# Kernel tuning notes

Measured on AMD Instinct MI355X. Metric: run time of the kernel, lower is better.

## Reference

```python
import jax, jax.numpy as jnp
import numpy as np

H = 1024
S = 8192
B = 1  # module's broadcast in the weighted-sum step only supports B == 1


def setup_inputs() -> dict:
    key = jax.random.key(0)
    k1, k2, k3 = jax.random.split(key, 3)
    scale = 1.0 / np.sqrt(H)
    enc_out = jax.random.normal(k1, (B, S, H), dtype=jnp.float32)
    w1 = jax.random.normal(k2, (H, H), dtype=jnp.float32) * scale  # nn.Linear weight [out,in]
    w2 = jax.random.normal(k3, (H, H), dtype=jnp.float32) * scale
    return {"enc_out": enc_out, "w1": w1, "w2": w2}


def reference(enc_out, w1, w2):
    # attn_weights = tanh(w1(enc_out)) @ w2(enc_out)^T  -> [B, S, S]
    q = jnp.tanh(jnp.einsum('bsh,oh->bso', enc_out, w1))
    k = jnp.einsum('bsh,oh->bso', enc_out, w2)
    scores = jnp.einsum('bih,bjh->bij', q, k)          # [B, S, S]
    attn = jax.nn.softmax(scores, axis=1)               # softmax over dim=1 (rows)
    # torch: sum over dim=1 of attn[B,S,S,1] * enc_out broadcast as [1,B,S,H].
    # For B==1 this equals enc_out[0,j,h] * sum_i attn[0,i,j]; avoid the
    # [B,S,S,H] intermediate the eager torch code materializes.
    col_sum = jnp.sum(attn, axis=1)                     # [B, S]
    context = col_sum[..., None] * enc_out              # [B, S, H]
    return context, attn
```

## Files before the change

### kernel.cpp

```cpp
#include <hip/hip_runtime.h>
#include <hip/hip_bf16.h>
#include <math.h>


typedef _Float16 half_t;
typedef _Float16 half8 __attribute__((ext_vector_type(8)));
typedef _Float16 half4 __attribute__((ext_vector_type(4)));
typedef float f32x4 __attribute__((ext_vector_type(4)));

#define S_DIM 8192
#define H_DIM 1024

__device__ __forceinline__ void gload16(const void* g, void* l) {
  __builtin_amdgcn_global_load_lds(
      (const __attribute__((address_space(1))) void*)g,
      (__attribute__((address_space(3))) void*)l, 16, 0, 0);
}

#define WAITVM(N) asm volatile("s_waitcnt vmcnt(" #N ")" ::: "memory")

__global__ void __launch_bounds__(256) k_cvt(const float* __restrict__ src,
                                             half_t* __restrict__ dst) {
  long g = (long)blockIdx.x * 256 + threadIdx.x;
  f32x4 x = ((const f32x4*)src)[g];
  half4 h;
#pragma unroll
  for (int e = 0; e < 4; ++e) h[e] = (half_t)x[e];
  ((half4*)dst)[g] = h;
}

#define GEMM_MAINLOOP_256(APTR, BPTR)                                          \
  __shared__ __align__(16) half_t As[4][8192];                                 \
  __shared__ __align__(16) half_t Bs[4][8192];                                 \
  const int tid = threadIdx.x;                                                 \
  const int lane = tid & 63;                                                   \
  const int quad = lane >> 4;                                                  \
  const int l15 = lane & 15;                                                   \
  const int wave = tid >> 6;                                                   \
  const int wm = wave >> 2;                                          \
  const int wn = wave & 3;                                           \
  int aoff[2], boff[2], loff[2];                                               \
  _Pragma("unroll") for (int t = 0; t < 2; ++t) {                              \
    int f8 = t * 512 + tid;                                       \
    int u = f8 >> 8;                                                 \
    int m = f8 & 255;                                                          \
    aoff[t] = (bm * 256 + m) * H_DIM + u * 8;                                  \
    boff[t] = (bn * 256 + m) * H_DIM + u * 8;                                  \
    loff[t] = f8 * 8;                                                          \
  }                                                                            \
  f32x4 acc[8][4];                                                             \
  _Pragma("unroll") for (int r = 0; r < 8; ++r)                                \
      _Pragma("unroll") for (int c = 0; c < 4; ++c)                            \
          acc[r][c] = (f32x4){0.f, 0.f, 0.f, 0.f};                             \
               \
  _Pragma("unroll") for (int pc = 0; pc < 3; ++pc)                             \
      _Pragma("unroll") for (int t = 0; t < 2; ++t) {                          \
    gload16(APTR + aoff[t] + pc * 32, &As[pc][loff[t]]);                       \
    gload16(BPTR + boff[t] + pc * 32, &Bs[pc][loff[t]]);                       \
  }                                                                            \
  const int abase = (quad * 256 + wm * 128 + l15) * 8;                         \
  const int bbase = (quad * 256 + wn * 64 + l15) * 8;                          \
  _Pragma("unroll 1") for (int ch = 0; ch < 32; ++ch) {                        \
    const int buf = ch & 3;                                                    \
    if (ch <= 29) { WAITVM(8); }           \
    else if (ch == 30) { WAITVM(4); }                                          \
    else { WAITVM(0); }                                                        \
    __builtin_amdgcn_s_barrier();                                              \
    asm volatile("" ::: "memory");        \
    if (ch + 3 < 32) {  \
      const int nb = (ch + 3) & 3;                                             \
      _Pragma("unroll") for (int t = 0; t < 2; ++t) {                          \
        gload16(APTR + aoff[t] + (ch + 3) * 32, &As[nb][loff[t]]);             \
        gload16(BPTR + boff[t] + (ch + 3) * 32, &Bs[nb][loff[t]]);             \
      }                                                                        \
    }                                                                          \
    half8 af[8], bf[4];                                                        \
    _Pragma("unroll") for (int r = 0; r < 8; ++r)                              \
        af[r] = *(const half8*)&As[buf][abase + r * 128];                      \
    _Pragma("unroll") for (int c = 0; c < 4; ++c)                              \
        bf[c] = *(const half8*)&Bs[buf][bbase + c * 128];                      \
    __builtin_amdgcn_s_setprio(1);                                             \
    _Pragma("unroll") for (int r = 0; r < 8; ++r)                              \
        _Pragma("unroll") for (int c = 0; c < 4; ++c)                          \
            acc[r][c] = __builtin_amdgcn_mfma_f32_16x16x32_f16(                \
                af[r], bf[c], acc[r][c], 0, 0, 0);                             \
    __builtin_amdgcn_s_setprio(0);                                             \
  }

__global__ void __launch_bounds__(512, 2) k_gemm_qk(const half_t* __restrict__ A,
                                                    const half_t* __restrict__ B,
                                                    half_t* __restrict__ Qh,
                                                    half_t* __restrict__ Kh) {
  const int bm = blockIdx.y;
  const int bn = blockIdx.x;
  GEMM_MAINLOOP_256(A, B)
  const int colb = bn * 256 + wn * 64;
  const int rowb = bm * 256 + wm * 128;
  const bool isQ = (bn < 4);
#pragma unroll
  for (int r = 0; r < 8; ++r) {
#pragma unroll
    for (int c = 0; c < 4; ++c) {
      int col = colb + c * 16 + l15;
      int row = rowb + r * 16 + quad * 4;
      if (isQ) {
#pragma unroll
        for (int v = 0; v < 4; ++v)
          Qh[(long)(row + v) * 1024 + col] = (half_t)tanhf(acc[r][c][v]);
      } else {
#pragma unroll
        for (int v = 0; v < 4; ++v)
          Kh[(long)(row + v) * 1024 + (col - 1024)] = (half_t)acc[r][c][v];
      }
    }
  }
}

template <bool FUSE_STATS>
__global__ void __launch_bounds__(512, 2) k_gemm_scores(const half_t* __restrict__ A,
                                                        const half_t* __restrict__ B,
                                                        float* __restrict__ out,
                                                        float* __restrict__ Pm,
                                                        float* __restrict__ Ps) {
  const int lin = blockIdx.x;
  const int patch = lin >> 6;
  const int local = lin & 63;
  const int bm = (patch >> 2) * 8 + (local >> 3);
  const int bn = (patch & 3) * 8 + (local & 7);
  GEMM_MAINLOOP_256(A, B)
  const int colb = bn * 256 + wn * 64;
  const int rowb = bm * 256 + wm * 128;
#pragma unroll
  for (int r = 0; r < 8; ++r) {
#pragma unroll
    for (int c = 0; c < 4; ++c) {
      int col = colb + c * 16 + l15;
      int row = rowb + r * 16 + quad * 4;
#pragma unroll
      for (int v = 0; v < 4; ++v) {
        out[(long)(row + v) * S_DIM + col] = acc[r][c][v];
      }
    }
  }
  if (FUSE_STATS) {
    float cmax[4], csum[4];
#pragma unroll
    for (int c = 0; c < 4; ++c) {
      float m = acc[0][c][0];
#pragma unroll
      for (int r = 0; r < 8; ++r)
#pragma unroll
        for (int v = 0; v < 4; ++v) m = fmaxf(m, acc[r][c][v]);
      m = fmaxf(m, __shfl_xor(m, 16, 64));
      m = fmaxf(m, __shfl_xor(m, 32, 64));
      cmax[c] = m;
      float s = 0.f;
#pragma unroll
      for (int r = 0; r < 8; ++r)
#pragma unroll
        for (int v = 0; v < 4; ++v) s += __expf(acc[r][c][v] - m);
      s += __shfl_xor(s, 16, 64);
      s += __shfl_xor(s, 32, 64);
      csum[c] = s;
    }
    float* sred = (float*)As;
    if (quad == 0) {
#pragma unroll
      for (int c = 0; c < 4; ++c) {
        int idx = (((wm * 4 + wn) * 4 + c) * 16 + l15) * 2;
        sred[idx] = cmax[c];
        sred[idx + 1] = csum[c];
      }
    }
    __syncthreads();
    if (wm == 0 && quad == 0) {
#pragma unroll
      for (int c = 0; c < 4; ++c) {
        int i0 = (((0 * 4 + wn) * 4 + c) * 16 + l15) * 2;
        int i1 = (((1 * 4 + wn) * 4 + c) * 16 + l15) * 2;
        float m0 = sred[i0], s0 = sred[i0 + 1];
        float m1 = sred[i1], s1 = sred[i1 + 1];
        float M = fmaxf(m0, m1);
        float Ssum = s0 * __expf(m0 - M) + s1 * __expf(m1 - M);
        int col = colb + c * 16 + l15;
        Pm[(long)bm * S_DIM + col] = M;
        Ps[(long)bm * S_DIM + col] = Ssum;
      }
    }
  }
}

__global__ void __launch_bounds__(256) k_colstats(const float* __restrict__ P,
                                                  float* __restrict__ Pm,
                                                  float* __restrict__ Ps) {
  const int c = threadIdx.x & 63;
  const int rg = threadIdx.x >> 6;
  const int j = blockIdx.x * 64 + c;
  const int seg = blockIdx.y;
  float m = -3.0e38f, s = 0.f;
  for (int t = 0; t < 256; ++t) {
    int i = seg * 1024 + t * 4 + rg;
    float x = P[(long)i * S_DIM + j];
    float mn = fmaxf(m, x);
    s = s * __expf(m - mn) + __expf(x - mn);
    m = mn;
  }
  __shared__ float sm[4][64];
  __shared__ float ss[4][64];
  sm[rg][c] = m;
  ss[rg][c] = s;
  __syncthreads();
  if (threadIdx.x < 64) {
    float mm = sm[0][c];
#pragma unroll
    for (int r = 1; r < 4; ++r) mm = fmaxf(mm, sm[r][c]);
    float sum = 0.f;
#pragma unroll
    for (int r = 0; r < 4; ++r) sum += ss[r][c] * __expf(sm[r][c] - mm);
    Pm[seg * S_DIM + j] = mm;
    Ps[seg * S_DIM + j] = sum;
  }
}

__global__ void __launch_bounds__(256) k_combine(const float* __restrict__ Pm,
                                                 const float* __restrict__ Ps,
                                                 float* __restrict__ Mcol,
                                                 float* __restrict__ Rcol,
                                                 int nseg) {
  int j = blockIdx.x * 256 + threadIdx.x;
  float m = Pm[j];
  for (int r = 1; r < nseg; ++r) m = fmaxf(m, Pm[(long)r * S_DIM + j]);
  float s = 0.f;
  for (int r = 0; r < nseg; ++r)
    s += Ps[(long)r * S_DIM + j] * __expf(Pm[(long)r * S_DIM + j] - m);
  Mcol[j] = m;
  Rcol[j] = 1.0f / s;
}

__global__ void __launch_bounds__(256) k_norm(float* __restrict__ P,
                                              const float* __restrict__ Mcol,
                                              const float* __restrict__ Rcol,
                                              const f32x4* __restrict__ enc,
                                              f32x4* __restrict__ ctx) {
  long b = blockIdx.x;
  if (b >= 65536) {
    long g = (b - 65536) * 256 + threadIdx.x;
    ctx[g] = enc[g];
    return;
  }
  long gid = b * 256 + threadIdx.x;
  int j4 = (int)(gid & 2047);
  f32x4 x = ((const f32x4*)P)[gid];
  f32x4 a = ((const f32x4*)Mcol)[j4];
  f32x4 r = ((const f32x4*)Rcol)[j4];
  f32x4 o;
#pragma unroll
  for (int e = 0; e < 4; ++e) o[e] = __expf(x[e] - a[e]) * r[e];
  ((f32x4*)P)[gid] = o;
}

extern "C" void kernel_launch(void* const* d_in, const int* in_sizes, int n_in,
                              void* d_out, int out_size, void* d_ws, size_t ws_size,
                              hipStream_t stream) {
  const float* enc = (const float*)d_in[0];
  const float* w1 = (const float*)d_in[1];
  const float* w2 = (const float*)d_in[2];

  float* out = (float*)d_out;
  float* ctx = out;
  float* attn = out + 8388608;

  half_t* Qh = (half_t*)ctx;
  half_t* Kh = Qh + 8388608;
  half_t* enc_h = (half_t*)attn;
  half_t* w_h = (half_t*)((char*)attn + 16777216);

  const bool fuse = ws_size >= (size_t)(32 + 32 + 2) * S_DIM * 4;
  const int nseg = fuse ? 32 : 8;
  char* ws = (char*)d_ws;
  float* Pm = (float*)ws;
  float* Ps = (float*)(ws + (size_t)nseg * S_DIM * 4);
  float* Mcol = (float*)(ws + (size_t)2 * nseg * S_DIM * 4);
  float* Rcol = Mcol + S_DIM;

  k_cvt<<<8192, 256, 0, stream>>>(enc, enc_h);
  k_cvt<<<1024, 256, 0, stream>>>(w1, w_h);
  k_cvt<<<1024, 256, 0, stream>>>(w2, w_h + 1048576);

  k_gemm_qk<<<dim3(8, 32), 512, 0, stream>>>(enc_h, w_h, Qh, Kh);

  if (fuse) {
    k_gemm_scores<true><<<1024, 512, 0, stream>>>(Qh, Kh, attn, Pm, Ps);
  } else {
    k_gemm_scores<false><<<1024, 512, 0, stream>>>(Qh, Kh, attn, Pm, Ps);
    k_colstats<<<dim3(128, 8), 256, 0, stream>>>(attn, Pm, Ps);
  }
  k_combine<<<32, 256, 0, stream>>>(Pm, Ps, Mcol, Rcol, nseg);

  k_norm<<<73728, 256, 0, stream>>>(attn, Mcol, Rcol, (const f32x4*)enc,
                                    (f32x4*)ctx);
}
```

Before: 785.7 us.

## Recompute score GEMM instead of materializing scores, and split mainloop into phases

```diff
diff --git a/kernel.cpp b/kernel.cpp
--- a/kernel.cpp
+++ b/kernel.cpp
@@ -1,5 +1,4 @@
 #include <hip/hip_runtime.h>
-#include <hip/hip_bf16.h>
 #include <math.h>
 
 
@@ -18,6 +17,12 @@
 }
 
 #define WAITVM(N) asm volatile("s_waitcnt vmcnt(" #N ")" ::: "memory")
+#define BAR()                      \
+  do {                             \
+    asm volatile("" ::: "memory"); \
+    __builtin_amdgcn_s_barrier();  \
+    asm volatile("" ::: "memory"); \
+  } while (0)
 
 __global__ void __launch_bounds__(256) k_cvt(const float* __restrict__ src,
                                              half_t* __restrict__ dst) {
@@ -29,7 +34,7 @@
   ((half4*)dst)[g] = h;
 }
 
-#define GEMM_MAINLOOP_256(APTR, BPTR)                                          \
+#define GEMM_MAINLOOP_8PH(APTR, BPTR)                                          \
   __shared__ __align__(16) half_t As[4][8192];                                 \
   __shared__ __align__(16) half_t Bs[4][8192];                                 \
   const int tid = threadIdx.x;                                                 \
@@ -41,50 +46,69 @@
   const int wn = wave & 3;                                           \
   int aoff[2], boff[2], loff[2];                                               \
   _Pragma("unroll") for (int t = 0; t < 2; ++t) {                              \
-    int f8 = t * 512 + tid;                                       \
-    int u = f8 >> 8;                                                 \
-    int m = f8 & 255;                                                          \
+    int f = t * 512 + tid;                                        \
+    int u = f >> 8;                                                  \
+    int m = f & 255;                                                           \
     aoff[t] = (bm * 256 + m) * H_DIM + u * 8;                                  \
     boff[t] = (bn * 256 + m) * H_DIM + u * 8;                                  \
-    loff[t] = f8 * 8;                                                          \
+    loff[t] = f * 8;                                                           \
   }                                                                            \
   f32x4 acc[8][4];                                                             \
   _Pragma("unroll") for (int r = 0; r < 8; ++r)                                \
       _Pragma("unroll") for (int c = 0; c < 4; ++c)                            \
           acc[r][c] = (f32x4){0.f, 0.f, 0.f, 0.f};                             \
-               \
-  _Pragma("unroll") for (int pc = 0; pc < 3; ++pc)                             \
-      _Pragma("unroll") for (int t = 0; t < 2; ++t) {                          \
-    gload16(APTR + aoff[t] + pc * 32, &As[pc][loff[t]]);                       \
-    gload16(BPTR + boff[t] + pc * 32, &Bs[pc][loff[t]]);                       \
+                      \
+  _Pragma("unroll") for (int pg = 0; pg < 3; ++pg) {                           \
+    _Pragma("unroll") for (int t = 0; t < 2; ++t)                              \
+        gload16(APTR + aoff[t] + pg * 32, &As[pg][loff[t]]);                   \
+    _Pragma("unroll") for (int t = 0; t < 2; ++t)                              \
+        gload16(BPTR + boff[t] + pg * 32, &Bs[pg][loff[t]]);                   \
   }                                                                            \
-  const int abase = (quad * 256 + wm * 128 + l15) * 8;                         \
-  const int bbase = (quad * 256 + wn * 64 + l15) * 8;                          \
-  _Pragma("unroll 1") for (int ch = 0; ch < 32; ++ch) {                        \
-    const int buf = ch & 3;                                                    \
-    if (ch <= 29) { WAITVM(8); }           \
-    else if (ch == 30) { WAITVM(4); }                                          \
-    else { WAITVM(0); }                                                        \
-    __builtin_amdgcn_s_barrier();                                              \
-    asm volatile("" ::: "memory");        \
-    if (ch + 3 < 32) {  \
-      const int nb = (ch + 3) & 3;                                             \
-      _Pragma("unroll") for (int t = 0; t < 2; ++t) {                          \
-        gload16(APTR + aoff[t] + (ch + 3) * 32, &As[nb][loff[t]]);             \
-        gload16(BPTR + boff[t] + (ch + 3) * 32, &Bs[nb][loff[t]]);             \
-      }                                                                        \
+  WAITVM(4);               \
+  BAR();                                                                       \
+  const int arow = (quad * 256 + wm * 128 + l15) * 8;                          \
+  const int brow = (quad * 256 + wn * 64 + l15) * 8;                           \
+  _Pragma("unroll 1") for (int g = 0; g < 32; ++g) {                           \
+    const half_t* Asl = As[g & 3];                                             \
+    const half_t* Bsl = Bs[g & 3];                                             \
+    half8 af[4], bf[4];                                                        \
+                             \
+    _Pragma("unroll") for (int r = 0; r < 4; ++r)                              \
+        af[r] = *(const half8*)&Asl[arow + r * 128];                           \
+    _Pragma("unroll") for (int c = 0; c < 4; ++c)                              \
+        bf[c] = *(const half8*)&Bsl[brow + c * 128];                           \
+    if (g + 3 < 32) {                 \
+      const int ns = (g + 3) & 3;                                              \
+      _Pragma("unroll") for (int t = 0; t < 2; ++t)                            \
+          gload16(APTR + aoff[t] + (g + 3) * 32, &As[ns][loff[t]]);            \
     }                                                                          \
-    half8 af[8], bf[4];                                                        \
-    _Pragma("unroll") for (int r = 0; r < 8; ++r)                              \
-        af[r] = *(const half8*)&As[buf][abase + r * 128];                      \
-    _Pragma("unroll") for (int c = 0; c < 4; ++c)                              \
-        bf[c] = *(const half8*)&Bs[buf][bbase + c * 128];                      \
+    BAR();                                                                     \
     __builtin_amdgcn_s_setprio(1);                                             \
-    _Pragma("unroll") for (int r = 0; r < 8; ++r)                              \
+    _Pragma("unroll") for (int r = 0; r < 4; ++r)                              \
         _Pragma("unroll") for (int c = 0; c < 4; ++c)                          \
             acc[r][c] = __builtin_amdgcn_mfma_f32_16x16x32_f16(                \
                 af[r], bf[c], acc[r][c], 0, 0, 0);                             \
     __builtin_amdgcn_s_setprio(0);                                             \
+    BAR();                                                                     \
+                   \
+    _Pragma("unroll") for (int r = 0; r < 4; ++r)                              \
+        af[r] = *(const half8*)&Asl[arow + (r + 4) * 128];                     \
+    if (g + 3 < 32) {                                   \
+      const int ns = (g + 3) & 3;                                              \
+      _Pragma("unroll") for (int t = 0; t < 2; ++t)                            \
+          gload16(BPTR + boff[t] + (g + 3) * 32, &Bs[ns][loff[t]]);            \
+    }                                                                          \
+    BAR();                                                                     \
+    __builtin_amdgcn_s_setprio(1);                                             \
+    _Pragma("unroll") for (int r = 0; r < 4; ++r)                              \
+        _Pragma("unroll") for (int c = 0; c < 4; ++c)                          \
+            acc[r + 4][c] = __builtin_amdgcn_mfma_f32_16x16x32_f16(            \
+                af[r], bf[c], acc[r + 4][c], 0, 0, 0);                         \
+    __builtin_amdgcn_s_setprio(0);                                             \
+    if (g & 1) {           \
+      if (g < 27) { WAITVM(4); } else { WAITVM(0); }                           \
+    }                                                                          \
+    BAR();                                                                     \
   }
 
 __global__ void __launch_bounds__(512, 2) k_gemm_qk(const half_t* __restrict__ A,
@@ -93,7 +117,7 @@
                                                     half_t* __restrict__ Kh) {
   const int bm = blockIdx.y;
   const int bn = blockIdx.x;
-  GEMM_MAINLOOP_256(A, B)
+  GEMM_MAINLOOP_8PH(A, B)
   const int colb = bn * 256 + wn * 64;
   const int rowb = bm * 256 + wm * 128;
   const bool isQ = (bn < 4);
@@ -116,147 +140,110 @@
   }
 }
 
-template <bool FUSE_STATS>
-__global__ void __launch_bounds__(512, 2) k_gemm_scores(const half_t* __restrict__ A,
-                                                        const half_t* __restrict__ B,
-                                                        float* __restrict__ out,
-                                                        float* __restrict__ Pm,
-                                                        float* __restrict__ Ps) {
+__global__ void __launch_bounds__(512, 2) k_stats(const half_t* __restrict__ A,
+                                                  const half_t* __restrict__ B,
+                                                  float* __restrict__ Pm,
+                                                  float* __restrict__ Ps) {
   const int lin = blockIdx.x;
   const int patch = lin >> 6;
   const int local = lin & 63;
   const int bm = (patch >> 2) * 8 + (local >> 3);
   const int bn = (patch & 3) * 8 + (local & 7);
-  GEMM_MAINLOOP_256(A, B)
+  GEMM_MAINLOOP_8PH(A, B)
   const int colb = bn * 256 + wn * 64;
-  const int rowb = bm * 256 + wm * 128;
-#pragma unroll
-  for (int r = 0; r < 8; ++r) {
+  float cmax[4], csum[4];
+#pragma unroll
+  for (int c = 0; c < 4; ++c) {
+    float m = acc[0][c][0];
+#pragma unroll
+    for (int r = 0; r < 8; ++r)
+#pragma unroll
+      for (int v = 0; v < 4; ++v) m = fmaxf(m, acc[r][c][v]);
+    m = fmaxf(m, __shfl_xor(m, 16, 64));
+    m = fmaxf(m, __shfl_xor(m, 32, 64));
+    cmax[c] = m;
+    float s = 0.f;
+#pragma unroll
+    for (int r = 0; r < 8; ++r)
+#pragma unroll
+      for (int v = 0; v < 4; ++v) s += __expf(acc[r][c][v] - m);
+    s += __shfl_xor(s, 16, 64);
+    s += __shfl_xor(s, 32, 64);
+    csum[c] = s;
+  }
+  float* sred = (float*)As;
+  if (quad == 0) {
 #pragma unroll
     for (int c = 0; c < 4; ++c) {
+      int idx = (((wm * 4 + wn) * 4 + c) * 16 + l15) * 2;
+      sred[idx] = cmax[c];
+      sred[idx + 1] = csum[c];
+    }
+  }
+  __syncthreads();
+  if (wm == 0 && quad == 0) {
+#pragma unroll
+    for (int c = 0; c < 4; ++c) {
+      int i0 = (((0 * 4 + wn) * 4 + c) * 16 + l15) * 2;
+      int i1 = (((1 * 4 + wn) * 4 + c) * 16 + l15) * 2;
+      float m0 = sred[i0], s0 = sred[i0 + 1];
+      float m1 = sred[i1], s1 = sred[i1 + 1];
+      float M = fmaxf(m0, m1);
+      float Ssum = s0 * __expf(m0 - M) + s1 * __expf(m1 - M);
       int col = colb + c * 16 + l15;
-      int row = rowb + r * 16 + quad * 4;
-#pragma unroll
-      for (int v = 0; v < 4; ++v) {
-        out[(long)(row + v) * S_DIM + col] = acc[r][c][v];
-      }
-    }
-  }
-  if (FUSE_STATS) {
-    float cmax[4], csum[4];
-#pragma unroll
-    for (int c = 0; c < 4; ++c) {
-      float m = acc[0][c][0];
-#pragma unroll
-      for (int r = 0; r < 8; ++r)
-#pragma unroll
-        for (int v = 0; v < 4; ++v) m = fmaxf(m, acc[r][c][v]);
-      m = fmaxf(m, __shfl_xor(m, 16, 64));
-      m = fmaxf(m, __shfl_xor(m, 32, 64));
-      cmax[c] = m;
-      float s = 0.f;
-#pragma unroll
-      for (int r = 0; r < 8; ++r)
-#pragma unroll
-        for (int v = 0; v < 4; ++v) s += __expf(acc[r][c][v] - m);
-      s += __shfl_xor(s, 16, 64);
-      s += __shfl_xor(s, 32, 64);
-      csum[c] = s;
-    }
-    float* sred = (float*)As;
-    if (quad == 0) {
-#pragma unroll
-      for (int c = 0; c < 4; ++c) {
-        int idx = (((wm * 4 + wn) * 4 + c) * 16 + l15) * 2;
-        sred[idx] = cmax[c];
-        sred[idx + 1] = csum[c];
-      }
-    }
-    __syncthreads();
-    if (wm == 0 && quad == 0) {
-#pragma unroll
-      for (int c = 0; c < 4; ++c) {
-        int i0 = (((0 * 4 + wn) * 4 + c) * 16 + l15) * 2;
-        int i1 = (((1 * 4 + wn) * 4 + c) * 16 + l15) * 2;
-        float m0 = sred[i0], s0 = sred[i0 + 1];
-        float m1 = sred[i1], s1 = sred[i1 + 1];
-        float M = fmaxf(m0, m1);
-        float Ssum = s0 * __expf(m0 - M) + s1 * __expf(m1 - M);
-        int col = colb + c * 16 + l15;
-        Pm[(long)bm * S_DIM + col] = M;
-        Ps[(long)bm * S_DIM + col] = Ssum;
-      }
-    }
-  }
-}
-
-__global__ void __launch_bounds__(256) k_colstats(const float* __restrict__ P,
-                                                  float* __restrict__ Pm,
-                                                  float* __restrict__ Ps) {
-  const int c = threadIdx.x & 63;
-  const int rg = threadIdx.x >> 6;
-  const int j = blockIdx.x * 64 + c;
-  const int seg = blockIdx.y;
-  float m = -3.0e38f, s = 0.f;
-  for (int t = 0; t < 256; ++t) {
-    int i = seg * 1024 + t * 4 + rg;
-    float x = P[(long)i * S_DIM + j];
-    float mn = fmaxf(m, x);
-    s = s * __expf(m - mn) + __expf(x - mn);
-    m = mn;
-  }
-  __shared__ float sm[4][64];
-  __shared__ float ss[4][64];
-  sm[rg][c] = m;
-  ss[rg][c] = s;
-  __syncthreads();
-  if (threadIdx.x < 64) {
-    float mm = sm[0][c];
-#pragma unroll
-    for (int r = 1; r < 4; ++r) mm = fmaxf(mm, sm[r][c]);
-    float sum = 0.f;
-#pragma unroll
-    for (int r = 0; r < 4; ++r) sum += ss[r][c] * __expf(sm[r][c] - mm);
-    Pm[seg * S_DIM + j] = mm;
-    Ps[seg * S_DIM + j] = sum;
+      Pm[(long)bm * S_DIM + col] = M;
+      Ps[(long)bm * S_DIM + col] = Ssum;
+    }
   }
 }
 
 __global__ void __launch_bounds__(256) k_combine(const float* __restrict__ Pm,
                                                  const float* __restrict__ Ps,
                                                  float* __restrict__ Mcol,
-                                                 float* __restrict__ Rcol,
-                                                 int nseg) {
+                                                 float* __restrict__ Rcol) {
   int j = blockIdx.x * 256 + threadIdx.x;
   float m = Pm[j];
-  for (int r = 1; r < nseg; ++r) m = fmaxf(m, Pm[(long)r * S_DIM + j]);
+  for (int r = 1; r < 32; ++r) m = fmaxf(m, Pm[(long)r * S_DIM + j]);
   float s = 0.f;
-  for (int r = 0; r < nseg; ++r)
+  for (int r = 0; r < 32; ++r)
     s += Ps[(long)r * S_DIM + j] * __expf(Pm[(long)r * S_DIM + j] - m);
   Mcol[j] = m;
   Rcol[j] = 1.0f / s;
 }
 
-__global__ void __launch_bounds__(256) k_norm(float* __restrict__ P,
-                                              const float* __restrict__ Mcol,
-                                              const float* __restrict__ Rcol,
-                                              const f32x4* __restrict__ enc,
-                                              f32x4* __restrict__ ctx) {
-  long b = blockIdx.x;
-  if (b >= 65536) {
-    long g = (b - 65536) * 256 + threadIdx.x;
-    ctx[g] = enc[g];
-    return;
-  }
-  long gid = b * 256 + threadIdx.x;
-  int j4 = (int)(gid & 2047);
-  f32x4 x = ((const f32x4*)P)[gid];
-  f32x4 a = ((const f32x4*)Mcol)[j4];
-  f32x4 r = ((const f32x4*)Rcol)[j4];
-  f32x4 o;
-#pragma unroll
-  for (int e = 0; e < 4; ++e) o[e] = __expf(x[e] - a[e]) * r[e];
-  ((f32x4*)P)[gid] = o;
+__global__ void __launch_bounds__(512, 2) k_attn(const half_t* __restrict__ A,
+                                                 const half_t* __restrict__ B,
+                                                 const float* __restrict__ Mcol,
+                                                 const float* __restrict__ Rcol,
+                                                 float* __restrict__ out) {
+  const int lin = blockIdx.x;
+  const int patch = lin >> 6;
+  const int local = lin & 63;
+  const int bm = (patch >> 2) * 8 + (local >> 3);
+  const int bn = (patch & 3) * 8 + (local & 7);
+  GEMM_MAINLOOP_8PH(A, B)
+  const int colb = bn * 256 + wn * 64;
+  const int rowb = bm * 256 + wm * 128;
+#pragma unroll
+  for (int c = 0; c < 4; ++c) {
+    int col = colb + c * 16 + l15;
+    float M = Mcol[col];
+    float R = Rcol[col];
+#pragma unroll
+    for (int r = 0; r < 8; ++r) {
+      int row = rowb + r * 16 + quad * 4;
+#pragma unroll
+      for (int v = 0; v < 4; ++v) {
+        out[(long)(row + v) * S_DIM + col] = __expf(acc[r][c][v] - M) * R;
+      }
+    }
+  }
+}
+
+__global__ void __launch_bounds__(256) k_ctx(const f32x4* __restrict__ enc,
+                                             f32x4* __restrict__ ctx) {
+  long g = (long)blockIdx.x * 256 + threadIdx.x;
+  ctx[g] = enc[g];
 }
 
 extern "C" void kernel_launch(void* const* d_in, const int* in_sizes, int n_in,
@@ -274,13 +261,9 @@
   half_t* Kh = Qh + 8388608;
   half_t* enc_h = (half_t*)attn;
   half_t* w_h = (half_t*)((char*)attn + 16777216);
-
-  const bool fuse = ws_size >= (size_t)(32 + 32 + 2) * S_DIM * 4;
-  const int nseg = fuse ? 32 : 8;
-  char* ws = (char*)d_ws;
-  float* Pm = (float*)ws;
-  float* Ps = (float*)(ws + (size_t)nseg * S_DIM * 4);
-  float* Mcol = (float*)(ws + (size_t)2 * nseg * S_DIM * 4);
+  float* Pm = attn + 8388608;
+  float* Ps = Pm + 32 * S_DIM;
+  float* Mcol = (float*)d_ws;
   float* Rcol = Mcol + S_DIM;
 
   k_cvt<<<8192, 256, 0, stream>>>(enc, enc_h);
@@ -289,14 +272,10 @@
 
   k_gemm_qk<<<dim3(8, 32), 512, 0, stream>>>(enc_h, w_h, Qh, Kh);
 
-  if (fuse) {
-    k_gemm_scores<true><<<1024, 512, 0, stream>>>(Qh, Kh, attn, Pm, Ps);
-  } else {
-    k_gemm_scores<false><<<1024, 512, 0, stream>>>(Qh, Kh, attn, Pm, Ps);
-    k_colstats<<<dim3(128, 8), 256, 0, stream>>>(attn, Pm, Ps);
-  }
-  k_combine<<<32, 256, 0, stream>>>(Pm, Ps, Mcol, Rcol, nseg);
-
-  k_norm<<<73728, 256, 0, stream>>>(attn, Mcol, Rcol, (const f32x4*)enc,
-                                    (f32x4*)ctx);
-}
+  k_stats<<<1024, 512, 0, stream>>>(Qh, Kh, Pm, Ps);
+  k_combine<<<32, 256, 0, stream>>>(Pm, Ps, Mcol, Rcol);
+
+  k_attn<<<1024, 512, 0, stream>>>(Qh, Kh, Mcol, Rcol, attn);
+
+  k_ctx<<<8192, 256, 0, stream>>>((const f32x4*)enc, (f32x4*)ctx);
+}
```

After: 725.0 us. 7.7% less time.
